# Kernel optimization log

Measured on AMD Instinct MI355X. Metric: run time of the kernel, lower is better.

## Reference

```python
import jax, jax.numpy as jnp
import numpy as np

N = 100000   # nodes
E = 1600000  # edges (avg degree 16)
D = 128      # in_channels
H = 128      # hidden_channels
C = 40       # n_classes


def setup_inputs() -> dict:
    key = jax.random.key(0)
    ks = jax.random.split(key, 6)
    x = jax.random.normal(ks[0], (N, D), dtype=jnp.float32)
    edge_index = jax.random.randint(ks[1], (2, E), 0, N, dtype=jnp.int32)
    glorot = lambda k, fi, fo: jax.random.normal(k, (fi, fo), jnp.float32) * (1.0 / np.sqrt(fi))
    return {
        "x": x,
        "edge_index": edge_index,
        "W0": glorot(ks[2], D, H), "b0": jnp.zeros((H,), jnp.float32),
        "W1": glorot(ks[3], H, H), "b1": jnp.zeros((H,), jnp.float32),
        "W2": glorot(ks[4], H, C), "b2": jnp.zeros((C,), jnp.float32),
    }


def reference(x, edge_index, W0, b0, W1, b1, W2, b2):
    n = x.shape[0]
    loop = jnp.arange(n, dtype=edge_index.dtype)
    src = jnp.concatenate([edge_index[0], loop])  # add self-loops (GCNConv default)
    dst = jnp.concatenate([edge_index[1], loop])
    # symmetric normalization D^-1/2 A D^-1/2
    deg = jax.ops.segment_sum(jnp.ones(src.shape[0], x.dtype), dst, num_segments=n)
    dinv = jnp.where(deg > 0, jax.lax.rsqrt(deg), 0.0)
    norm = dinv[src] * dinv[dst]  # [E+N]

    def conv(h, W, b):
        h = h @ W                          # linear transform first (small d)
        msg = h[src] * norm[:, None]       # gather + scale
        return jax.ops.segment_sum(msg, dst, num_segments=n) + b  # scatter-add

    h = jax.nn.relu(conv(x, W0, b0))   # dropout omitted (eval mode)
    h = jax.nn.relu(conv(h, W1, b1))
    return conv(h, W2, b2)             # [N, C] logits; wrapper returns (out, None)
```

## Files before the change

### kernel.cpp

```cpp
#include <hip/hip_runtime.h>
#include <hip/hip_bf16.h>
#include <hip/hip_fp16.h>


#define CAP 64
#define CAPSH 6
#define NXCD 8

typedef _Float16 f16x8 __attribute__((ext_vector_type(8)));
typedef float f32x4 __attribute__((ext_vector_type(4)));

union U16B {
    int4 i;
    f16x8 h;
};


__global__ void init_cursor(int* cursor, int n) {
    int i = blockIdx.x * blockDim.x + threadIdx.x;
    int stride = gridDim.x * blockDim.x;
    for (; i < n; i += stride) cursor[i] = i << CAPSH;
}

__global__ __launch_bounds__(256) void scatter_kernel(const int* __restrict__ src,
                                                      const int* __restrict__ dst, int E,
                                                      int* cursor, int* col, int nper) {
    int p = blockIdx.x & (NXCD - 1);
    int blkInGrp = blockIdx.x >> 3;
    int nGrpBlk = gridDim.x >> 3;
    int lo = p * nper, hi = lo + nper;
    int tid0 = blkInGrp * 256 + threadIdx.x;
    int stride = nGrpBlk * 256;
    int E4 = E >> 2;
    const int4* dst4 = (const int4*)dst;
    const int4* src4 = (const int4*)src;
    for (int e = tid0; e < E4; e += stride) {
        int4 d = dst4[e];
        int4 s = src4[e];
        if (d.x >= lo && d.x < hi) {
            int pos = atomicAdd(&cursor[d.x], 1);
            if (pos - (d.x << CAPSH) < CAP) col[pos] = s.x;
        }
        if (d.y >= lo && d.y < hi) {
            int pos = atomicAdd(&cursor[d.y], 1);
            if (pos - (d.y << CAPSH) < CAP) col[pos] = s.y;
        }
        if (d.z >= lo && d.z < hi) {
            int pos = atomicAdd(&cursor[d.z], 1);
            if (pos - (d.z << CAPSH) < CAP) col[pos] = s.z;
        }
        if (d.w >= lo && d.w < hi) {
            int pos = atomicAdd(&cursor[d.w], 1);
            if (pos - (d.w << CAPSH) < CAP) col[pos] = s.w;
        }
    }
    for (int e = (E4 << 2) + tid0; e < E; e += stride) {
        int d = dst[e];
        if (d >= lo && d < hi) {
            int pos = atomicAdd(&cursor[d], 1);
            if (pos - (d << CAPSH) < CAP) col[pos] = src[e];
        }
    }
}

__global__ void dinv_kernel(const int* __restrict__ cursor, float* dinv, int n) {
    int i = blockIdx.x * blockDim.x + threadIdx.x;
    int stride = gridDim.x * blockDim.x;
    for (; i < n; i += stride) {
        int deg = cursor[i] - (i << CAPSH);
        dinv[i] = rsqrtf(1.0f + (float)deg);
    }
}


__global__ void f32_to_f16_vec(const float* __restrict__ in, __half* __restrict__ out, int n4) {
    int i = blockIdx.x * blockDim.x + threadIdx.x;
    int stride = gridDim.x * blockDim.x;
    const float4* in4 = (const float4*)in;
    float2* out2 = (float2*)out;
    for (; i < n4; i += stride) {
        float4 v = in4[i];
        union {
            __half2 h2[2];
            float2 f2;
        } u;
        u.h2[0] = __floats2half2_rn(v.x, v.y);
        u.h2[1] = __floats2half2_rn(v.z, v.w);
        out2[i] = u.f2;
    }
}

__global__ void pack_w(const float* __restrict__ W, __half* __restrict__ Wf) {
    int tid = blockIdx.x * blockDim.x + threadIdx.x;
    int stride = gridDim.x * blockDim.x;
    for (int idx = tid; idx < 16384; idx += stride) {
        int j = idx & 7;
        int l = (idx >> 3) & 63;
        int ct = (idx >> 9) & 7;
        int ks = idx >> 12;
        int k = ks * 32 + ((l >> 4) << 3) + j;
        int c = ct * 16 + (l & 15);
        Wf[idx] = __float2half(W[k * 128 + c]);
    }
}


__global__ __launch_bounds__(256) void gemm_mfma_128(const __half* __restrict__ A,
                                                     const __half* __restrict__ Wf,
                                                     __half* __restrict__ C, int n) {
    __shared__ int4 lds[2048];
    int tid = threadIdx.x;
    const int4* wsrc = (const int4*)Wf;
    for (int i = tid; i < 2048; i += 256) lds[i] = wsrc[i];
    __syncthreads();

    int lane = tid & 63;
    int wave = tid >> 6;
    int rsub = lane & 15;
    int kgrp = (lane >> 4) * 8;
    int ntiles = (n + 63) >> 6;

    for (int tile = blockIdx.x; tile < ntiles; tile += gridDim.x) {
        int row0 = tile * 64 + wave * 16;
        int arow = row0 + rsub;
        bool valid = arow < n;
        f16x8 afrag[4];
#pragma unroll
        for (int ks = 0; ks < 4; ++ks) {
            U16B u;
            u.i = valid ? *(const int4*)(A + (size_t)arow * 128 + ks * 32 + kgrp)
                        : int4{0, 0, 0, 0};
            afrag[ks] = u.h;
        }
        f32x4 acc[8];
#pragma unroll
        for (int ct = 0; ct < 8; ++ct) acc[ct] = {0.f, 0.f, 0.f, 0.f};
#pragma unroll
        for (int ks = 0; ks < 4; ++ks) {
#pragma unroll
            for (int ct = 0; ct < 8; ++ct) {
                U16B b;
                b.i = lds[(ks * 8 + ct) * 64 + lane];
                acc[ct] = __builtin_amdgcn_mfma_f32_16x16x32_f16(afrag[ks], b.h, acc[ct], 0, 0, 0);
            }
        }
        int crow0 = row0 + ((lane >> 4) << 2);
#pragma unroll
        for (int ct = 0; ct < 8; ++ct) {
#pragma unroll
            for (int j = 0; j < 4; ++j) {
                int r = crow0 + j;
                if (r < n) C[(size_t)r * 128 + ct * 16 + rsub] = __float2half(acc[ct][j]);
            }
        }
    }
}


__device__ __forceinline__ float4 ld4h(const __half* A, size_t idx) {
    union {
        float2 f2;
        __half2 h2[2];
    } u;
    u.f2 = ((const float2*)A)[idx];
    float2 lo = __half22float2(u.h2[0]);
    float2 hi = __half22float2(u.h2[1]);
    return float4{lo.x, lo.y, hi.x, hi.y};
}

__global__ __launch_bounds__(256) void gemm_k128_m40(const __half* __restrict__ A,
                                                     const float* __restrict__ W,
                                                     __half* __restrict__ C, int n) {
    __shared__ float Ws[128 * 40];
    int tid = threadIdx.x;
    for (int j = tid; j < 128 * 40; j += 256) Ws[j] = W[j];
    __syncthreads();
    int lane = tid & 63;
    bool act = lane < 40;
    int cl = act ? lane : 0;
    int wid = (blockIdx.x * 256 + tid) >> 6;
    int nw = (gridDim.x * 256) >> 6;
    for (int r = wid; r < n; r += nw) {
        const __half* Arow = A + (size_t)r * 128;
        float acc = 0.f;
#pragma unroll 8
        for (int k4 = 0; k4 < 32; ++k4) {
            float4 a = ld4h(Arow, k4);
            acc = fmaf(a.x, Ws[(k4 * 4 + 0) * 40 + cl], acc);
            acc = fmaf(a.y, Ws[(k4 * 4 + 1) * 40 + cl], acc);
            acc = fmaf(a.z, Ws[(k4 * 4 + 2) * 40 + cl], acc);
            acc = fmaf(a.w, Ws[(k4 * 4 + 3) * 40 + cl], acc);
        }
        if (act) C[(size_t)r * 40 + lane] = __float2half_rn(acc);
    }
}


__global__ __launch_bounds__(256) void agg128(const __half* __restrict__ t,
                                              const int* __restrict__ col,
                                              const int* __restrict__ cursor,
                                              const float* __restrict__ dinv,
                                              const float* __restrict__ bias,
                                              __half* __restrict__ out, int n, int dorelu) {
    int lane = threadIdx.x & 63;
    int wid = (blockIdx.x * 256 + threadIdx.x) >> 6;
    int nw = (gridDim.x * 256) >> 6;
    const __half2* t2 = (const __half2*)t;
    float2 b = ((const float2*)bias)[lane];
    for (int i = wid; i < n; i += nw) {
        float di = dinv[i];
        float dii = di * di;
        float2 sl = __half22float2(t2[(size_t)i * 64 + lane]);
        float2 acc;
        acc.x = sl.x * dii;
        acc.y = sl.y * dii;
        int e = i << CAPSH;
        int eend = cursor[i];
        int emax = e + CAP;
        if (eend > emax) eend = emax;
        for (; e + 3 < eend; e += 4) {
            int s0 = col[e], s1 = col[e + 1], s2 = col[e + 2], s3 = col[e + 3];
            float w0 = dinv[s0] * di;
            float w1 = dinv[s1] * di;
            float w2 = dinv[s2] * di;
            float w3 = dinv[s3] * di;
            float2 v0 = __half22float2(t2[(size_t)s0 * 64 + lane]);
            float2 v1 = __half22float2(t2[(size_t)s1 * 64 + lane]);
            float2 v2 = __half22float2(t2[(size_t)s2 * 64 + lane]);
            float2 v3 = __half22float2(t2[(size_t)s3 * 64 + lane]);
            acc.x = fmaf(v0.x, w0, acc.x);
            acc.y = fmaf(v0.y, w0, acc.y);
            acc.x = fmaf(v1.x, w1, acc.x);
            acc.y = fmaf(v1.y, w1, acc.y);
            acc.x = fmaf(v2.x, w2, acc.x);
            acc.y = fmaf(v2.y, w2, acc.y);
            acc.x = fmaf(v3.x, w3, acc.x);
            acc.y = fmaf(v3.y, w3, acc.y);
        }
        for (; e < eend; ++e) {
            int s0 = col[e];
            float w0 = dinv[s0] * di;
            float2 v0 = __half22float2(t2[(size_t)s0 * 64 + lane]);
            acc.x = fmaf(v0.x, w0, acc.x);
            acc.y = fmaf(v0.y, w0, acc.y);
        }
        acc.x += b.x;
        acc.y += b.y;
        if (dorelu) {
            acc.x = fmaxf(acc.x, 0.f);
            acc.y = fmaxf(acc.y, 0.f);
        }
        ((__half2*)out)[(size_t)i * 64 + lane] = __floats2half2_rn(acc.x, acc.y);
    }
}

__global__ __launch_bounds__(256) void agg40(const __half* __restrict__ t,
                                             const int* __restrict__ col,
                                             const int* __restrict__ cursor,
                                             const float* __restrict__ dinv,
                                             const float* __restrict__ bias,
                                             float* __restrict__ out, int n) {
    int lane = threadIdx.x & 63;
    bool act = lane < 40;
    int cl = act ? lane : 0;
    int wid = (blockIdx.x * 256 + threadIdx.x) >> 6;
    int nw = (gridDim.x * 256) >> 6;
    float b = bias[cl];
    for (int i = wid; i < n; i += nw) {
        float di = dinv[i];
        float acc = __half2float(t[(size_t)i * 40 + cl]) * di * di;
        int e = i << CAPSH;
        int eend = cursor[i];
        int emax = e + CAP;
        if (eend > emax) eend = emax;
        for (; e + 3 < eend; e += 4) {
            int s0 = col[e], s1 = col[e + 1], s2 = col[e + 2], s3 = col[e + 3];
            float w0 = dinv[s0] * di;
            float w1 = dinv[s1] * di;
            float w2 = dinv[s2] * di;
            float w3 = dinv[s3] * di;
            float v0 = __half2float(t[(size_t)s0 * 40 + cl]);
            float v1 = __half2float(t[(size_t)s1 * 40 + cl]);
            float v2 = __half2float(t[(size_t)s2 * 40 + cl]);
            float v3 = __half2float(t[(size_t)s3 * 40 + cl]);
            acc = fmaf(v0, w0, acc);
            acc = fmaf(v1, w1, acc);
            acc = fmaf(v2, w2, acc);
            acc = fmaf(v3, w3, acc);
        }
        for (; e < eend; ++e) {
            int s0 = col[e];
            float w0 = dinv[s0] * di;
            acc = fmaf(__half2float(t[(size_t)s0 * 40 + cl]), w0, acc);
        }
        if (act) out[(size_t)i * 40 + lane] = acc + b;
    }
}


extern "C" void kernel_launch(void* const* d_in, const int* in_sizes, int n_in,
                              void* d_out, int out_size, void* d_ws, size_t ws_size,
                              hipStream_t stream) {
    const float* x = (const float*)d_in[0];
    const int* ei = (const int*)d_in[1];
    const float* W0 = (const float*)d_in[2];
    const float* b0 = (const float*)d_in[3];
    const float* W1 = (const float*)d_in[4];
    const float* b1 = (const float*)d_in[5];
    const float* W2 = (const float*)d_in[6];
    const float* b2 = (const float*)d_in[7];
    float* out = (float*)d_out;

    const int N = in_sizes[0] / 128;
    const int E = in_sizes[1] / 2;
    const int* src = ei;
    const int* dst = ei + E;

    __half* X16 = (__half*)d_ws;
    __half* T = X16 + (size_t)N * 128;
    __half* H = T + (size_t)N * 128;
    float* dinv = (float*)(H + (size_t)N * 128);
    int* cursor = (int*)(dinv + N);
    int* col = cursor + N;
    __half* Wf0 = (__half*)(col + (size_t)N * CAP);
    __half* Wf1 = Wf0 + 16384;

    init_cursor<<<512, 256, 0, stream>>>(cursor, N);
    int nper = (N + NXCD - 1) / NXCD;
    scatter_kernel<<<2048, 256, 0, stream>>>(src, dst, E, cursor, col, nper);
    dinv_kernel<<<512, 256, 0, stream>>>(cursor, dinv, N);

    f32_to_f16_vec<<<2048, 256, 0, stream>>>(x, X16, N * 32);
    pack_w<<<16, 256, 0, stream>>>(W0, Wf0);
    pack_w<<<16, 256, 0, stream>>>(W1, Wf1);

    int ntile = (N + 63) >> 6;
    int ngrid = ntile < 1024 ? ntile : 1024;

    gemm_mfma_128<<<ngrid, 256, 0, stream>>>(X16, Wf0, T, N);
    agg128<<<2048, 256, 0, stream>>>(T, col, cursor, dinv, b0, H, N, 1);

    gemm_mfma_128<<<ngrid, 256, 0, stream>>>(H, Wf1, T, N);
    agg128<<<2048, 256, 0, stream>>>(T, col, cursor, dinv, b1, H, N, 1);

    __half* T40 = T;
    gemm_k128_m40<<<2048, 256, 0, stream>>>(H, W2, T40, N);
    agg40<<<2048, 256, 0, stream>>>(T40, col, cursor, dinv, b2, out, N);
}
```

Measured before the change: 495.9 us.

## Fuse fp32-to-fp16 conversion into first GEMM and use MFMA for final layer

New measurement: 424.3 us. -14.4%, faster.

```diff
diff --git a/kernel.cpp b/kernel.cpp
--- a/kernel.cpp
+++ b/kernel.cpp
@@ -73,45 +73,51 @@
 }
 
 
-__global__ void f32_to_f16_vec(const float* __restrict__ in, __half* __restrict__ out, int n4) {
-    int i = blockIdx.x * blockDim.x + threadIdx.x;
-    int stride = gridDim.x * blockDim.x;
-    const float4* in4 = (const float4*)in;
-    float2* out2 = (float2*)out;
-    for (; i < n4; i += stride) {
-        float4 v = in4[i];
-        union {
-            __half2 h2[2];
-            float2 f2;
-        } u;
-        u.h2[0] = __floats2half2_rn(v.x, v.y);
-        u.h2[1] = __floats2half2_rn(v.z, v.w);
-        out2[i] = u.f2;
-    }
-}
-
+template <int NC, int CT>
 __global__ void pack_w(const float* __restrict__ W, __half* __restrict__ Wf) {
     int tid = blockIdx.x * blockDim.x + threadIdx.x;
     int stride = gridDim.x * blockDim.x;
-    for (int idx = tid; idx < 16384; idx += stride) {
+    const int total = 4 * CT * 64 * 8;
+    for (int idx = tid; idx < total; idx += stride) {
         int j = idx & 7;
         int l = (idx >> 3) & 63;
-        int ct = (idx >> 9) & 7;
-        int ks = idx >> 12;
+        int ct = (idx >> 9) % CT;
+        int ks = idx / (CT * 512);
         int k = ks * 32 + ((l >> 4) << 3) + j;
         int c = ct * 16 + (l & 15);
-        Wf[idx] = __float2half(W[k * 128 + c]);
-    }
-}
-
-
-__global__ __launch_bounds__(256) void gemm_mfma_128(const __half* __restrict__ A,
-                                                     const __half* __restrict__ Wf,
-                                                     __half* __restrict__ C, int n) {
-    __shared__ int4 lds[2048];
+        Wf[idx] = (c < NC) ? __float2half(W[k * NC + c]) : __half(0);
+    }
+}
+
+
+__device__ __forceinline__ f16x8 lda_frag(const __half* p) {
+    U16B u;
+    u.i = *(const int4*)p;
+    return u.h;
+}
+__device__ __forceinline__ f16x8 lda_frag(const float* p) {
+    float4 a = ((const float4*)p)[0];
+    float4 b = ((const float4*)p)[1];
+    f16x8 h;
+    h[0] = (_Float16)a.x; h[1] = (_Float16)a.y; h[2] = (_Float16)a.z; h[3] = (_Float16)a.w;
+    h[4] = (_Float16)b.x; h[5] = (_Float16)b.y; h[6] = (_Float16)b.z; h[7] = (_Float16)b.w;
+    return h;
+}
+__device__ __forceinline__ f16x8 zfrag() {
+    U16B u;
+    u.i = int4{0, 0, 0, 0};
+    return u.h;
+}
+
+
+template <typename TA, int NC, int CT>
+__global__ __launch_bounds__(256) void gemm_mfma(const TA* __restrict__ A,
+                                                 const __half* __restrict__ Wf,
+                                                 __half* __restrict__ C, int n) {
+    __shared__ int4 lds[4 * CT * 64];
     int tid = threadIdx.x;
     const int4* wsrc = (const int4*)Wf;
-    for (int i = tid; i < 2048; i += 256) lds[i] = wsrc[i];
+    for (int i = tid; i < 4 * CT * 64; i += 256) lds[i] = wsrc[i];
     __syncthreads();
 
     int lane = tid & 63;
@@ -126,72 +132,31 @@
         bool valid = arow < n;
         f16x8 afrag[4];
 #pragma unroll
+        for (int ks = 0; ks < 4; ++ks)
+            afrag[ks] = valid ? lda_frag(A + (size_t)arow * 128 + ks * 32 + kgrp) : zfrag();
+        f32x4 acc[CT];
+#pragma unroll
+        for (int ct = 0; ct < CT; ++ct) acc[ct] = {0.f, 0.f, 0.f, 0.f};
+#pragma unroll
         for (int ks = 0; ks < 4; ++ks) {
-            U16B u;
-            u.i = valid ? *(const int4*)(A + (size_t)arow * 128 + ks * 32 + kgrp)
-                        : int4{0, 0, 0, 0};
-            afrag[ks] = u.h;
-        }
-        f32x4 acc[8];
-#pragma unroll
-        for (int ct = 0; ct < 8; ++ct) acc[ct] = {0.f, 0.f, 0.f, 0.f};
-#pragma unroll
-        for (int ks = 0; ks < 4; ++ks) {
-#pragma unroll
-            for (int ct = 0; ct < 8; ++ct) {
+#pragma unroll
+            for (int ct = 0; ct < CT; ++ct) {
                 U16B b;
-                b.i = lds[(ks * 8 + ct) * 64 + lane];
+                b.i = lds[(ks * CT + ct) * 64 + lane];
                 acc[ct] = __builtin_amdgcn_mfma_f32_16x16x32_f16(afrag[ks], b.h, acc[ct], 0, 0, 0);
             }
         }
         int crow0 = row0 + ((lane >> 4) << 2);
 #pragma unroll
-        for (int ct = 0; ct < 8; ++ct) {
+        for (int ct = 0; ct < CT; ++ct) {
+            int c = ct * 16 + rsub;
+            if (c >= NC) continue;
 #pragma unroll
             for (int j = 0; j < 4; ++j) {
                 int r = crow0 + j;
-                if (r < n) C[(size_t)r * 128 + ct * 16 + rsub] = __float2half(acc[ct][j]);
+                if (r < n) C[(size_t)r * NC + c] = __float2half(acc[ct][j]);
             }
         }
-    }
-}
-
-
-__device__ __forceinline__ float4 ld4h(const __half* A, size_t idx) {
-    union {
-        float2 f2;
-        __half2 h2[2];
-    } u;
-    u.f2 = ((const float2*)A)[idx];
-    float2 lo = __half22float2(u.h2[0]);
-    float2 hi = __half22float2(u.h2[1]);
-    return float4{lo.x, lo.y, hi.x, hi.y};
-}
-
-__global__ __launch_bounds__(256) void gemm_k128_m40(const __half* __restrict__ A,
-                                                     const float* __restrict__ W,
-                                                     __half* __restrict__ C, int n) {
-    __shared__ float Ws[128 * 40];
-    int tid = threadIdx.x;
-    for (int j = tid; j < 128 * 40; j += 256) Ws[j] = W[j];
-    __syncthreads();
-    int lane = tid & 63;
-    bool act = lane < 40;
-    int cl = act ? lane : 0;
-    int wid = (blockIdx.x * 256 + tid) >> 6;
-    int nw = (gridDim.x * 256) >> 6;
-    for (int r = wid; r < n; r += nw) {
-        const __half* Arow = A + (size_t)r * 128;
-        float acc = 0.f;
-#pragma unroll 8
-        for (int k4 = 0; k4 < 32; ++k4) {
-            float4 a = ld4h(Arow, k4);
-            acc = fmaf(a.x, Ws[(k4 * 4 + 0) * 40 + cl], acc);
-            acc = fmaf(a.y, Ws[(k4 * 4 + 1) * 40 + cl], acc);
-            acc = fmaf(a.z, Ws[(k4 * 4 + 2) * 40 + cl], acc);
-            acc = fmaf(a.w, Ws[(k4 * 4 + 3) * 40 + cl], acc);
-        }
-        if (act) C[(size_t)r * 40 + lane] = __float2half_rn(acc);
     }
 }
 
@@ -316,34 +281,34 @@
     const int* src = ei;
     const int* dst = ei + E;
 
-    __half* X16 = (__half*)d_ws;
-    __half* T = X16 + (size_t)N * 128;
+    __half* T = (__half*)d_ws;
     __half* H = T + (size_t)N * 128;
     float* dinv = (float*)(H + (size_t)N * 128);
     int* cursor = (int*)(dinv + N);
     int* col = cursor + N;
     __half* Wf0 = (__half*)(col + (size_t)N * CAP);
     __half* Wf1 = Wf0 + 16384;
+    __half* Wf2 = Wf1 + 16384;
 
     init_cursor<<<512, 256, 0, stream>>>(cursor, N);
     int nper = (N + NXCD - 1) / NXCD;
     scatter_kernel<<<2048, 256, 0, stream>>>(src, dst, E, cursor, col, nper);
     dinv_kernel<<<512, 256, 0, stream>>>(cursor, dinv, N);
 
-    f32_to_f16_vec<<<2048, 256, 0, stream>>>(x, X16, N * 32);
-    pack_w<<<16, 256, 0, stream>>>(W0, Wf0);
-    pack_w<<<16, 256, 0, stream>>>(W1, Wf1);
+    pack_w<128, 8><<<16, 256, 0, stream>>>(W0, Wf0);
+    pack_w<128, 8><<<16, 256, 0, stream>>>(W1, Wf1);
+    pack_w<40, 3><<<8, 256, 0, stream>>>(W2, Wf2);
 
     int ntile = (N + 63) >> 6;
     int ngrid = ntile < 1024 ? ntile : 1024;
 
-    gemm_mfma_128<<<ngrid, 256, 0, stream>>>(X16, Wf0, T, N);
+    gemm_mfma<float, 128, 8><<<ngrid, 256, 0, stream>>>(x, Wf0, T, N);
     agg128<<<2048, 256, 0, stream>>>(T, col, cursor, dinv, b0, H, N, 1);
 
-    gemm_mfma_128<<<ngrid, 256, 0, stream>>>(H, Wf1, T, N);
+    gemm_mfma<__half, 128, 8><<<ngrid, 256, 0, stream>>>(H, Wf1, T, N);
     agg128<<<2048, 256, 0, stream>>>(T, col, cursor, dinv, b1, H, N, 1);
 
     __half* T40 = T;
-    gemm_k128_m40<<<2048, 256, 0, stream>>>(H, W2, T40, N);
+    gemm_mfma<__half, 40, 3><<<ngrid, 256, 0, stream>>>(H, Wf2, T40, N);
     agg40<<<2048, 256, 0, stream>>>(T40, col, cursor, dinv, b2, out, N);
 }
```
